# Optimization experiments

Measured on AMD Instinct MI355X. Metric: run time of the kernel, lower is better.

## Reference

```python
import jax, jax.numpy as jnp
import numpy as np

N_NODES = 100000
N_EDGES = 600000
D_IN = 128
D_HID = 128
NB_LAYERS = 3
EPS = 1e-5  # torch LayerNorm default


def setup_inputs() -> dict:
    key = jax.random.key(0)
    ks = jax.random.split(key, 12)
    x = jax.random.normal(ks[0], (N_NODES, D_IN), dtype=jnp.float32)
    edge_index = jax.random.randint(ks[1], (2, N_EDGES), 0, N_NODES, dtype=jnp.int32)
    # MLP sizes: [2*D_IN, D_HID, D_HID, D_HID, 1]
    sizes = [2 * D_IN] + [D_HID] * NB_LAYERS + [1]
    inp = {"x": x, "edge_index": edge_index}
    for i in range(len(sizes) - 1):
        scale = 1.0 / np.sqrt(sizes[i]).astype(np.float32)
        inp[f"W{i}"] = jax.random.normal(ks[2 + i], (sizes[i], sizes[i + 1]), dtype=jnp.float32) * scale
        inp[f"b{i}"] = jnp.zeros((sizes[i + 1],), dtype=jnp.float32)
    for i in range(NB_LAYERS):
        inp[f"g{i}"] = jnp.ones((D_HID,), dtype=jnp.float32)      # LayerNorm gamma
        inp[f"beta{i}"] = jnp.zeros((D_HID,), dtype=jnp.float32)  # LayerNorm beta
    return inp


def _layernorm(h, g, b):
    mu = jnp.mean(h, axis=-1, keepdims=True)
    var = jnp.var(h, axis=-1, keepdims=True)
    return (h - mu) * jax.lax.rsqrt(var + EPS) * g + b


def reference(x, edge_index, W0, b0, W1, b1, W2, b2, W3, b3, g0, beta0, g1, beta1, g2, beta2):
    start, end = edge_index[0], edge_index[1]
    # gather node pairs and concat -> [E, 2*D_IN]
    h = jnp.concatenate([x[start], x[end]], axis=1)
    for W, b, g, be in ((W0, b0, g0, beta0), (W1, b1, g1, beta1), (W2, b2, g2, beta2)):
        h = jnp.tanh(_layernorm(h @ W + b, g, be))
    return (h @ W3 + b3).squeeze(-1)  # [E]
```

## Files before the change

kernel.cpp:

```cpp
#include <hip/hip_runtime.h>
#include <hip/hip_bf16.h>


typedef float f32x4 __attribute__((ext_vector_type(4)));
typedef __bf16 bf16x8 __attribute__((ext_vector_type(8)));
typedef unsigned int u32x4 __attribute__((ext_vector_type(4)));

#define MFMA16(a, b, c) __builtin_amdgcn_mfma_f32_16x16x32_bf16((a), (b), (c), 0, 0, 0)
#define TWO_LOG2E 2.885390081777927f

static __device__ __forceinline__ unsigned short bf16bits(float f) {
  __bf16 h = (__bf16)f;
  return __builtin_bit_cast(unsigned short, h);
}

static __device__ __forceinline__ unsigned pack2(float a, float b) {
  return (unsigned)bf16bits(a) | ((unsigned)bf16bits(b) << 16);
}

static __device__ __forceinline__ float tanh_fast2(float z) {
#if __has_builtin(__builtin_amdgcn_exp2f)
  const float ex = __builtin_amdgcn_exp2f(z);
#else
  const float ex = exp2f(z);
#endif
  return 1.0f - 2.0f * __builtin_amdgcn_rcpf(ex + 1.0f);
}

static __device__ __forceinline__ void gload_lds16(const void* g, void* l) {
  __builtin_amdgcn_global_load_lds(
      (const __attribute__((address_space(1))) void*)g,
      (__attribute__((address_space(3))) void*)l, 16, 0, 0);
}

static __device__ __forceinline__ int permk(int k) {
  const int j = k & 7, g = (k >> 3) & 3;
  return (k & ~31) | ((j >> 2) << 4) | (g << 2) | (j & 3);
}

__global__ void prep_x(const float* __restrict__ x,
                       unsigned short* __restrict__ xb, int n8) {
  int gid = blockIdx.x * blockDim.x + threadIdx.x;
  const int stride = gridDim.x * blockDim.x;
  for (int i = gid; i < n8; i += stride) {
    const float4 a = ((const float4*)x)[i * 2];
    const float4 b = ((const float4*)x)[i * 2 + 1];
    u32x4 o;
    o[0] = pack2(a.x, a.y); o[1] = pack2(a.z, a.w);
    o[2] = pack2(b.x, b.y); o[3] = pack2(b.z, b.w);
    ((u32x4*)xb)[i] = o;
  }
}

__global__ void prep_w(const float* __restrict__ W0, const float* __restrict__ W1,
                       const float* __restrict__ W2,
                       const float* __restrict__ B0, const float* __restrict__ G0,
                       const float* __restrict__ Q0,
                       const float* __restrict__ B1, const float* __restrict__ G1,
                       const float* __restrict__ Q1,
                       const float* __restrict__ B2, const float* __restrict__ G2,
                       const float* __restrict__ Q2,
                       const float* __restrict__ W3,
                       unsigned short* __restrict__ wt, float* __restrict__ pp) {
  const int t = blockIdx.x;
  const int tid = threadIdx.x;
  if (t == 8) {
    for (int i = tid; i < 1280; i += 256) {
      const int a = i >> 7, o = i & 127;
      float v;
      switch (a) {
        case 0: v = B0[o]; break;
        case 1: v = G0[o] * TWO_LOG2E; break;
        case 2: v = Q0[o] * TWO_LOG2E; break;
        case 3: v = B1[o]; break;
        case 4: v = G1[o] * TWO_LOG2E; break;
        case 5: v = Q1[o] * TWO_LOG2E; break;
        case 6: v = B2[o]; break;
        case 7: v = G2[o] * TWO_LOG2E; break;
        case 8: v = Q2[o] * TWO_LOG2E; break;
        default: v = W3[o]; break;
      }
      pp[i] = v;
    }
    return;
  }
  const float* src; int kbase; int perm;
  if (t < 4)      { src = W0; kbase = t * 64;      perm = 0; }
  else if (t < 6) { src = W1; kbase = (t - 4) * 64; perm = 1; }
  else            { src = W2; kbase = (t - 6) * 64; perm = 1; }
  char* base = (char*)wt + t * 16384;
  const int col = tid & 127;
  const int kb  = (tid >> 7) << 1;
  #pragma unroll
  for (int i = 0; i < 16; ++i) {
    const int kl = kb + (i << 2);
    const int k0 = kbase + kl;
    const int c0 = perm ? permk(k0) : k0;
    const float wa = src[c0 * 128 + col];
    const float wb = src[(c0 + 1) * 128 + col];
    const unsigned pk = pack2(wa, wb);
    const int off = ((col * 64 + kl) * 2) ^ ((col & 7) << 4);
    *(unsigned*)(base + off) = pk;
  }
}

#define P_B0 0
#define P_G0 128
#define P_Q0 256
#define P_B1 384
#define P_G1 512
#define P_Q1 640
#define P_B2 768
#define P_G2 896
#define P_Q2 1024
#define P_W3 1152

template <int XB>
__global__ __launch_bounds__(256, 3) void edge_mlp(
    const float* __restrict__ x, const int* __restrict__ ei,
    const float* __restrict__ B3,
    const unsigned short* __restrict__ wt, const float* __restrict__ pp,
    const unsigned short* __restrict__ xbp,
    float* __restrict__ out, int nE)
{
  __shared__ __align__(16) char lds[32768 + 5120];
  float* plds = (float*)(lds + 32768);
  const int tid  = threadIdx.x;
  const int lane = tid & 63;
  const int wv   = tid >> 6;
  const int e    = lane & 15;
  const int g    = lane >> 4;

  const int wbase = blockIdx.x * 128 + wv * 32;
  const int e0 = wbase + e;
  const int e1 = wbase + 16 + e;
  const int ec0 = e0 < nE ? e0 : nE - 1;
  const int ec1 = e1 < nE ? e1 : nE - 1;
  const int ns0 = ei[ec0], ne0 = ei[nE + ec0];
  const int ns1 = ei[ec1], ne1 = ei[nE + ec1];

  auto stageW = [&](int t, int buf) {
    #pragma unroll
    for (int c = 0; c < 4; ++c) {
      const int o = wv * 4096 + c * 1024;
      gload_lds16((const char*)wt + t * 16384 + o + lane * 16,
                  lds + buf * 16384 + o);
    }
  };

  auto loadW = [&](int buf, int m, int kl) -> bf16x8 {
    const int col = m * 16 + e;
    const int off = ((col * 64 + kl) * 2) ^ ((col & 7) << 4);
    return *(const bf16x8*)(lds + buf * 16384 + off);
  };

  auto loadX = [&](int node, int ko) -> bf16x8 {
    if (XB) {
      return *(const bf16x8*)(xbp + (size_t)node * 128 + ko);
    } else {
      const float* src = x + (size_t)node * 128 + ko;
      const float4 ua = *(const float4*)(src);
      const float4 ub = *(const float4*)(src + 4);
      bf16x8 a;
      a[0] = (__bf16)ua.x; a[1] = (__bf16)ua.y; a[2] = (__bf16)ua.z; a[3] = (__bf16)ua.w;
      a[4] = (__bf16)ub.x; a[5] = (__bf16)ub.y; a[6] = (__bf16)ub.z; a[7] = (__bf16)ub.w;
      return a;
    }
  };

  auto ldslab = [&](int u0, bf16x8* dst) {
    #pragma unroll
    for (int du = 0; du < 2; ++du) {
      const int u = u0 + du;
      const int ko = (u & 3) * 32 + g * 8;
      dst[du * 2 + 0] = loadX(u < 4 ? ns0 : ne0, ko);
      dst[du * 2 + 1] = loadX(u < 4 ? ns1 : ne1, ko);
    }
  };

  f32x4 acc[8][2];

  auto initAcc = [&](int pb) {
    #pragma unroll
    for (int m = 0; m < 8; ++m) {
      const f32x4 bq = *(const f32x4*)(plds + pb + m * 16 + g * 4);
      acc[m][0] = bq; acc[m][1] = bq;
    }
  };

  auto l0mfma = [&](const bf16x8* xf, int buf) {
    #pragma unroll
    for (int du = 0; du < 2; ++du) {
      const int kl = du * 32 + g * 8;
      #pragma unroll
      for (int m = 0; m < 8; ++m) {
        const bf16x8 wf = loadW(buf, m, kl);
        acc[m][0] = MFMA16(wf, xf[du * 2 + 0], acc[m][0]);
        acc[m][1] = MFMA16(wf, xf[du * 2 + 1], acc[m][1]);
      }
    }
  };

  unsigned p0[2][8], p1[2][8];

  auto epi = [&](int pg, int pq) {
    #pragma unroll
    for (int j = 0; j < 2; ++j) {
      float s1a = 0.f, s1b = 0.f, s2a = 0.f, s2b = 0.f;
      #pragma unroll
      for (int m = 0; m < 8; m += 2) {
        #pragma unroll
        for (int r = 0; r < 4; ++r) {
          const float ta = acc[m][j][r];
          const float tb = acc[m + 1][j][r];
          s1a += ta; s1b += tb;
          s2a = __builtin_fmaf(ta, ta, s2a);
          s2b = __builtin_fmaf(tb, tb, s2b);
        }
      }
      float s1 = s1a + s1b, s2 = s2a + s2b;
      s1 += __shfl_xor(s1, 16); s2 += __shfl_xor(s2, 16);
      s1 += __shfl_xor(s1, 32); s2 += __shfl_xor(s2, 32);
      const float mu  = s1 * 0.0078125f;
      const float inv = __builtin_amdgcn_rsqf(s2 * 0.0078125f - mu * mu + 1e-5f);
      const float nm  = -mu * inv;
      #pragma unroll
      for (int m = 0; m < 8; ++m) {
        const f32x4 gq = *(const f32x4*)(plds + pg + m * 16 + g * 4);
        const f32x4 qq = *(const f32x4*)(plds + pq + m * 16 + g * 4);
        float th[4];
        #pragma unroll
        for (int r = 0; r < 4; ++r) {
          const float an = __builtin_fmaf(acc[m][j][r], inv, nm);
          const float z  = __builtin_fmaf(an, gq[r], qq[r]);
          th[r] = tanh_fast2(z);
        }
        p0[j][m] = pack2(th[0], th[1]);
        p1[j][m] = pack2(th[2], th[3]);
      }
    }
  };

  auto lstep = [&](int u0, int buf) {
    #pragma unroll
    for (int du = 0; du < 2; ++du) {
      const int u = u0 + du;
      const int kl = du * 32 + g * 8;
      u32x4 w0, w1;
      w0[0] = p0[0][2 * u];     w0[1] = p1[0][2 * u];
      w0[2] = p0[0][2 * u + 1]; w0[3] = p1[0][2 * u + 1];
      w1[0] = p0[1][2 * u];     w1[1] = p1[1][2 * u];
      w1[2] = p0[1][2 * u + 1]; w1[3] = p1[1][2 * u + 1];
      const bf16x8 bf0 = __builtin_bit_cast(bf16x8, w0);
      const bf16x8 bf1 = __builtin_bit_cast(bf16x8, w1);
      #pragma unroll
      for (int m = 0; m < 8; ++m) {
        const bf16x8 wf = loadW(buf, m, kl);
        acc[m][0] = MFMA16(wf, bf0, acc[m][0]);
        acc[m][1] = MFMA16(wf, bf1, acc[m][1]);
      }
    }
  };

  bf16x8 xra[4], xrb[4];
  stageW(0, 0);
  for (int i = tid; i < 1280; i += 256) plds[i] = pp[i];
  ldslab(0, xra);
  __syncthreads();

  initAcc(P_B0);
  stageW(1, 1); ldslab(2, xrb); l0mfma(xra, 0); __syncthreads();
  stageW(2, 0); ldslab(4, xra); l0mfma(xrb, 1); __syncthreads();
  stageW(3, 1); ldslab(6, xrb); l0mfma(xra, 0); __syncthreads();
  stageW(4, 0); l0mfma(xrb, 1); __syncthreads();
  stageW(5, 1);
  epi(P_G0, P_Q0); initAcc(P_B1); lstep(0, 0); __syncthreads();
  stageW(6, 0);
  lstep(2, 1); __syncthreads();
  stageW(7, 1);
  epi(P_G1, P_Q1); initAcc(P_B2); lstep(0, 0); __syncthreads();
  lstep(2, 1);

  const float b3v = B3[0];
  #pragma unroll
  for (int j = 0; j < 2; ++j) {
    float s1a = 0.f, s1b = 0.f, s2a = 0.f, s2b = 0.f;
    #pragma unroll
    for (int m = 0; m < 8; m += 2) {
      #pragma unroll
      for (int r = 0; r < 4; ++r) {
        const float ta = acc[m][j][r];
        const float tb = acc[m + 1][j][r];
        s1a += ta; s1b += tb;
        s2a = __builtin_fmaf(ta, ta, s2a);
        s2b = __builtin_fmaf(tb, tb, s2b);
      }
    }
    float s1 = s1a + s1b, s2 = s2a + s2b;
    s1 += __shfl_xor(s1, 16); s2 += __shfl_xor(s2, 16);
    s1 += __shfl_xor(s1, 32); s2 += __shfl_xor(s2, 32);
    const float mu  = s1 * 0.0078125f;
    const float inv = __builtin_amdgcn_rsqf(s2 * 0.0078125f - mu * mu + 1e-5f);
    const float nm  = -mu * inv;
    float d = 0.f;
    #pragma unroll
    for (int m = 0; m < 8; ++m) {
      const f32x4 gq  = *(const f32x4*)(plds + P_G2 + m * 16 + g * 4);
      const f32x4 qq  = *(const f32x4*)(plds + P_Q2 + m * 16 + g * 4);
      const f32x4 w3q = *(const f32x4*)(plds + P_W3 + m * 16 + g * 4);
      #pragma unroll
      for (int r = 0; r < 4; ++r) {
        const float an = __builtin_fmaf(acc[m][j][r], inv, nm);
        const float z  = __builtin_fmaf(an, gq[r], qq[r]);
        d = __builtin_fmaf(tanh_fast2(z), w3q[r], d);
      }
    }
    d += __shfl_xor(d, 16);
    d += __shfl_xor(d, 32);
    const int eid = wbase + j * 16 + e;
    if (g == 0 && eid < nE) out[eid] = d + b3v;
  }
}

extern "C" void kernel_launch(void* const* d_in, const int* in_sizes, int n_in,
                              void* d_out, int out_size, void* d_ws, size_t ws_size,
                              hipStream_t stream) {
  const float* x  = (const float*)d_in[0];
  const int*   ei = (const int*)d_in[1];
  const float* W0 = (const float*)d_in[2];
  const float* B0 = (const float*)d_in[3];
  const float* W1 = (const float*)d_in[4];
  const float* B1 = (const float*)d_in[5];
  const float* W2 = (const float*)d_in[6];
  const float* B2 = (const float*)d_in[7];
  const float* W3 = (const float*)d_in[8];
  const float* B3 = (const float*)d_in[9];
  const float* G0 = (const float*)d_in[10];
  const float* Q0 = (const float*)d_in[11];
  const float* G1 = (const float*)d_in[12];
  const float* Q1 = (const float*)d_in[13];
  const float* G2 = (const float*)d_in[14];
  const float* Q2 = (const float*)d_in[15];
  float* out = (float*)d_out;

  const int nX = in_sizes[0];
  const int nE = in_sizes[1] / 2;
  const int blocks = (nE + 127) / 128;

  const size_t xb_bytes = ((size_t)nX * 2 + 255) & ~(size_t)255;
  const int use_xb = (ws_size >= xb_bytes + 131072 + 5120) ? 1 : 0;

  unsigned short* xbp = (unsigned short*)d_ws;
  unsigned short* wt  = use_xb ? (unsigned short*)((char*)d_ws + xb_bytes)
                               : (unsigned short*)d_ws;
  float* pp = (float*)((char*)wt + 131072);

  hipLaunchKernelGGL(prep_w, dim3(9), dim3(256), 0, stream,
                     W0, W1, W2, B0, G0, Q0, B1, G1, Q1, B2, G2, Q2, W3, wt, pp);
  if (use_xb) {
    hipLaunchKernelGGL(prep_x, dim3(1024), dim3(256), 0, stream, x, xbp, nX / 8);
    hipLaunchKernelGGL(edge_mlp<1>, dim3(blocks), dim3(256), 0, stream,
                       x, ei, B3, wt, pp, xbp, out, nE);
  } else {
    hipLaunchKernelGGL(edge_mlp<0>, dim3(blocks), dim3(256), 0, stream,
                       x, ei, B3, wt, pp, xbp, out, nE);
  }
}
```

Measured before the change: 150.4 us.

## Process 16 edges per wave instead of 32 to raise occupancy

Each wave now handles one 16-edge tile instead of two, which halves the accumulator and packed-activation registers. Launch bounds rise from 3 to 4 blocks per CU, and the grid doubles to 64 edges per block. The X prefetch slab is dropped, so node features are loaded inline inside each layer-0 step instead of being software-pipelined ahead. The trade-off is that every weight fragment read from LDS now feeds only one MFMA instead of two, and the full weight set is staged through LDS twice as often across the grid.

```diff
diff --git a/kernel.cpp b/kernel.cpp
--- a/kernel.cpp
+++ b/kernel.cpp
@@ -116,7 +116,7 @@
 #define P_W3 1152
 
 template <int XB>
-__global__ __launch_bounds__(256, 3) void edge_mlp(
+__global__ __launch_bounds__(256, 4) void edge_mlp(
     const float* __restrict__ x, const int* __restrict__ ei,
     const float* __restrict__ B3,
     const unsigned short* __restrict__ wt, const float* __restrict__ pp,
@@ -131,13 +131,10 @@
   const int e    = lane & 15;
   const int g    = lane >> 4;
 
-  const int wbase = blockIdx.x * 128 + wv * 32;
+  const int wbase = blockIdx.x * 64 + wv * 16;
   const int e0 = wbase + e;
-  const int e1 = wbase + 16 + e;
   const int ec0 = e0 < nE ? e0 : nE - 1;
-  const int ec1 = e1 < nE ? e1 : nE - 1;
   const int ns0 = ei[ec0], ne0 = ei[nE + ec0];
-  const int ns1 = ei[ec1], ne1 = ei[nE + ec1];
 
   auto stageW = [&](int t, int buf) {
     #pragma unroll
@@ -168,76 +165,63 @@
     }
   };
 
-  auto ldslab = [&](int u0, bf16x8* dst) {
+  f32x4 acc[8];
+
+  auto initAcc = [&](int pb) {
+    #pragma unroll
+    for (int m = 0; m < 8; ++m)
+      acc[m] = *(const f32x4*)(plds + pb + m * 16 + g * 4);
+  };
+
+  auto l0step = [&](int u0, int buf) {
     #pragma unroll
     for (int du = 0; du < 2; ++du) {
       const int u = u0 + du;
       const int ko = (u & 3) * 32 + g * 8;
-      dst[du * 2 + 0] = loadX(u < 4 ? ns0 : ne0, ko);
-      dst[du * 2 + 1] = loadX(u < 4 ? ns1 : ne1, ko);
-    }
-  };
-
-  f32x4 acc[8][2];
-
-  auto initAcc = [&](int pb) {
-    #pragma unroll
-    for (int m = 0; m < 8; ++m) {
-      const f32x4 bq = *(const f32x4*)(plds + pb + m * 16 + g * 4);
-      acc[m][0] = bq; acc[m][1] = bq;
-    }
-  };
-
-  auto l0mfma = [&](const bf16x8* xf, int buf) {
-    #pragma unroll
-    for (int du = 0; du < 2; ++du) {
+      const bf16x8 xf = loadX(u < 4 ? ns0 : ne0, ko);
       const int kl = du * 32 + g * 8;
       #pragma unroll
       for (int m = 0; m < 8; ++m) {
         const bf16x8 wf = loadW(buf, m, kl);
-        acc[m][0] = MFMA16(wf, xf[du * 2 + 0], acc[m][0]);
-        acc[m][1] = MFMA16(wf, xf[du * 2 + 1], acc[m][1]);
-      }
-    }
-  };
-
-  unsigned p0[2][8], p1[2][8];
+        acc[m] = MFMA16(wf, xf, acc[m]);
+      }
+    }
+  };
+
+  unsigned p0[8], p1[8];
 
   auto epi = [&](int pg, int pq) {
-    #pragma unroll
-    for (int j = 0; j < 2; ++j) {
-      float s1a = 0.f, s1b = 0.f, s2a = 0.f, s2b = 0.f;
-      #pragma unroll
-      for (int m = 0; m < 8; m += 2) {
-        #pragma unroll
-        for (int r = 0; r < 4; ++r) {
-          const float ta = acc[m][j][r];
-          const float tb = acc[m + 1][j][r];
-          s1a += ta; s1b += tb;
-          s2a = __builtin_fmaf(ta, ta, s2a);
-          s2b = __builtin_fmaf(tb, tb, s2b);
-        }
-      }
-      float s1 = s1a + s1b, s2 = s2a + s2b;
-      s1 += __shfl_xor(s1, 16); s2 += __shfl_xor(s2, 16);
-      s1 += __shfl_xor(s1, 32); s2 += __shfl_xor(s2, 32);
-      const float mu  = s1 * 0.0078125f;
-      const float inv = __builtin_amdgcn_rsqf(s2 * 0.0078125f - mu * mu + 1e-5f);
-      const float nm  = -mu * inv;
-      #pragma unroll
-      for (int m = 0; m < 8; ++m) {
-        const f32x4 gq = *(const f32x4*)(plds + pg + m * 16 + g * 4);
-        const f32x4 qq = *(const f32x4*)(plds + pq + m * 16 + g * 4);
-        float th[4];
-        #pragma unroll
-        for (int r = 0; r < 4; ++r) {
-          const float an = __builtin_fmaf(acc[m][j][r], inv, nm);
-          const float z  = __builtin_fmaf(an, gq[r], qq[r]);
-          th[r] = tanh_fast2(z);
-        }
-        p0[j][m] = pack2(th[0], th[1]);
-        p1[j][m] = pack2(th[2], th[3]);
-      }
+    float s1a = 0.f, s1b = 0.f, s2a = 0.f, s2b = 0.f;
+    #pragma unroll
+    for (int m = 0; m < 8; m += 2) {
+      #pragma unroll
+      for (int r = 0; r < 4; ++r) {
+        const float ta = acc[m][r];
+        const float tb = acc[m + 1][r];
+        s1a += ta; s1b += tb;
+        s2a = __builtin_fmaf(ta, ta, s2a);
+        s2b = __builtin_fmaf(tb, tb, s2b);
+      }
+    }
+    float s1 = s1a + s1b, s2 = s2a + s2b;
+    s1 += __shfl_xor(s1, 16); s2 += __shfl_xor(s2, 16);
+    s1 += __shfl_xor(s1, 32); s2 += __shfl_xor(s2, 32);
+    const float mu  = s1 * 0.0078125f;
+    const float inv = __builtin_amdgcn_rsqf(s2 * 0.0078125f - mu * mu + 1e-5f);
+    const float nm  = -mu * inv;
+    #pragma unroll
+    for (int m = 0; m < 8; ++m) {
+      const f32x4 gq = *(const f32x4*)(plds + pg + m * 16 + g * 4);
+      const f32x4 qq = *(const f32x4*)(plds + pq + m * 16 + g * 4);
+      float th[4];
+      #pragma unroll
+      for (int r = 0; r < 4; ++r) {
+        const float an = __builtin_fmaf(acc[m][r], inv, nm);
+        const float z  = __builtin_fmaf(an, gq[r], qq[r]);
+        th[r] = tanh_fast2(z);
+      }
+      p0[m] = pack2(th[0], th[1]);
+      p1[m] = pack2(th[2], th[3]);
     }
   };
 
@@ -246,33 +230,27 @@
     for (int du = 0; du < 2; ++du) {
       const int u = u0 + du;
       const int kl = du * 32 + g * 8;
-      u32x4 w0, w1;
-      w0[0] = p0[0][2 * u];     w0[1] = p1[0][2 * u];
-      w0[2] = p0[0][2 * u + 1]; w0[3] = p1[0][2 * u + 1];
-      w1[0] = p0[1][2 * u];     w1[1] = p1[1][2 * u];
-      w1[2] = p0[1][2 * u + 1]; w1[3] = p1[1][2 * u + 1];
-      const bf16x8 bf0 = __builtin_bit_cast(bf16x8, w0);
-      const bf16x8 bf1 = __builtin_bit_cast(bf16x8, w1);
+      u32x4 w;
+      w[0] = p0[2 * u];     w[1] = p1[2 * u];
+      w[2] = p0[2 * u + 1]; w[3] = p1[2 * u + 1];
+      const bf16x8 bfv = __builtin_bit_cast(bf16x8, w);
       #pragma unroll
       for (int m = 0; m < 8; ++m) {
         const bf16x8 wf = loadW(buf, m, kl);
-        acc[m][0] = MFMA16(wf, bf0, acc[m][0]);
-        acc[m][1] = MFMA16(wf, bf1, acc[m][1]);
-      }
-    }
-  };
-
-  bf16x8 xra[4], xrb[4];
+        acc[m] = MFMA16(wf, bfv, acc[m]);
+      }
+    }
+  };
+
   stageW(0, 0);
   for (int i = tid; i < 1280; i += 256) plds[i] = pp[i];
-  ldslab(0, xra);
   __syncthreads();
 
   initAcc(P_B0);
-  stageW(1, 1); ldslab(2, xrb); l0mfma(xra, 0); __syncthreads();
-  stageW(2, 0); ldslab(4, xra); l0mfma(xrb, 1); __syncthreads();
-  stageW(3, 1); ldslab(6, xrb); l0mfma(xra, 0); __syncthreads();
-  stageW(4, 0); l0mfma(xrb, 1); __syncthreads();
+  stageW(1, 1); l0step(0, 0); __syncthreads();
+  stageW(2, 0); l0step(2, 1); __syncthreads();
+  stageW(3, 1); l0step(4, 0); __syncthreads();
+  stageW(4, 0); l0step(6, 1); __syncthreads();
   stageW(5, 1);
   epi(P_G0, P_Q0); initAcc(P_B1); lstep(0, 0); __syncthreads();
   stageW(6, 0);
@@ -282,15 +260,14 @@
   lstep(2, 1);
 
   const float b3v = B3[0];
-  #pragma unroll
-  for (int j = 0; j < 2; ++j) {
+  {
     float s1a = 0.f, s1b = 0.f, s2a = 0.f, s2b = 0.f;
     #pragma unroll
     for (int m = 0; m < 8; m += 2) {
       #pragma unroll
       for (int r = 0; r < 4; ++r) {
-        const float ta = acc[m][j][r];
-        const float tb = acc[m + 1][j][r];
+        const float ta = acc[m][r];
+        const float tb = acc[m + 1][r];
         s1a += ta; s1b += tb;
         s2a = __builtin_fmaf(ta, ta, s2a);
         s2b = __builtin_fmaf(tb, tb, s2b);
@@ -310,14 +287,14 @@
       const f32x4 w3q = *(const f32x4*)(plds + P_W3 + m * 16 + g * 4);
       #pragma unroll
       for (int r = 0; r < 4; ++r) {
-        const float an = __builtin_fmaf(acc[m][j][r], inv, nm);
+        const float an = __builtin_fmaf(acc[m][r], inv, nm);
         const float z  = __builtin_fmaf(an, gq[r], qq[r]);
         d = __builtin_fmaf(tanh_fast2(z), w3q[r], d);
       }
     }
     d += __shfl_xor(d, 16);
     d += __shfl_xor(d, 32);
-    const int eid = wbase + j * 16 + e;
+    const int eid = wbase + e;
     if (g == 0 && eid < nE) out[eid] = d + b3v;
   }
 }
@@ -345,7 +322,7 @@
 
   const int nX = in_sizes[0];
   const int nE = in_sizes[1] / 2;
-  const int blocks = (nE + 127) / 128;
+  const int blocks = (nE + 63) / 64;
 
   const size_t xb_bytes = ((size_t)nX * 2 + 255) & ~(size_t)255;
   const int use_xb = (ws_size >= xb_bytes + 131072 + 5120) ? 1 : 0;
```

After: 160.2 us. +6.5%, slower.
